# Kernel tuning notes

Hardware: AMD Instinct MI355X
Metric: run time of the kernel (lower is better)

The kernel has to match this reference:

```python
import jax, jax.numpy as jnp
import numpy as np
from jax import lax

B, S, T, E, H, V = 32, 64, 48, 512, 1024, 32000
PAD = 0


def lstm_cell(x, h, c, W_ih, W_hh, b_ih, b_hh):
    # PyTorch gate order: i, f, g, o
    gates = x @ W_ih.T + b_ih + h @ W_hh.T + b_hh
    i, f, g, o = jnp.split(gates, 4, axis=-1)
    c = jax.nn.sigmoid(f) * c + jax.nn.sigmoid(i) * jnp.tanh(g)
    h = jax.nn.sigmoid(o) * jnp.tanh(c)
    return h, c


def setup_inputs() -> dict:
    key = jax.random.key(0)
    ks = jax.random.split(key, 24)
    sc = 0.02
    n = lambda k, shape: jax.random.normal(k, shape, jnp.float32) * sc
    src_emb = n(ks[0], (V, E)).at[PAD].set(0.0)
    tgt_emb = n(ks[1], (V, E)).at[PAD].set(0.0)
    inp = {
        "input_sequences": jax.random.randint(ks[2], (B, S), 0, V),
        "target_sequences": jax.random.randint(ks[3], (B, T), 0, V),
        "src_emb": src_emb,
        "tgt_emb": tgt_emb,
        "enc_Wih_f": n(ks[4], (4 * H, E)),
        "enc_Whh_f": n(ks[5], (4 * H, H)),
        "enc_bih_f": n(ks[6], (4 * H,)),
        "enc_bhh_f": n(ks[7], (4 * H,)),
        "enc_Wih_b": n(ks[8], (4 * H, E)),
        "enc_Whh_b": n(ks[9], (4 * H, H)),
        "enc_bih_b": n(ks[10], (4 * H,)),
        "enc_bhh_b": n(ks[11], (4 * H,)),
        "dec_Wih": n(ks[12], (4 * H, E + H)),
        "dec_Whh": n(ks[13], (4 * H, H)),
        "dec_bih": n(ks[14], (4 * H,)),
        "dec_bhh": n(ks[15], (4 * H,)),
        "W_init_h": n(ks[16], (H, 2 * H)),
        "W_init_c": n(ks[17], (H, 2 * H)),
        "W_att": n(ks[18], (H, 2 * H)),
        "W_comb": n(ks[19], (H, 3 * H)),
        "W_proj": n(ks[20], (V, H)),
    }
    return inp


def reference(input_sequences, target_sequences, src_emb, tgt_emb,
              enc_Wih_f, enc_Whh_f, enc_bih_f, enc_bhh_f,
              enc_Wih_b, enc_Whh_b, enc_bih_b, enc_bhh_b,
              dec_Wih, dec_Whh, dec_bih, dec_bhh,
              W_init_h, W_init_c, W_att, W_comb, W_proj):
    bsz = input_sequences.shape[0]
    x_src = src_emb[input_sequences.T]  # (S, B, E) time-major

    def make_enc_step(W_ih, W_hh, b_ih, b_hh):
        def step(carry, x):
            h, c = carry
            h, c = lstm_cell(x, h, c, W_ih, W_hh, b_ih, b_hh)
            return (h, c), h
        return step

    h0 = jnp.zeros((bsz, H), x_src.dtype)
    c0 = jnp.zeros((bsz, H), x_src.dtype)
    # bidirectional encoder
    (hf, cf), hs_f = lax.scan(make_enc_step(enc_Wih_f, enc_Whh_f, enc_bih_f, enc_bhh_f), (h0, c0), x_src)
    (hb, cb), hs_b = lax.scan(make_enc_step(enc_Wih_b, enc_Whh_b, enc_bih_b, enc_bhh_b), (h0, c0), x_src[::-1])
    enc_h = jnp.concatenate([hs_f, hs_b[::-1]], axis=-1).transpose(1, 0, 2)  # (B, S, 2H)
    last_hidden = jnp.concatenate([hf, hb], axis=-1)  # (B, 2H)
    last_cell = jnp.concatenate([cf, cb], axis=-1)

    dec_h0 = last_hidden @ W_init_h.T
    dec_c0 = last_cell @ W_init_c.T
    enc_att = enc_h @ W_att.T  # (B, S, H)

    x_tgt = tgt_emb[target_sequences.T]  # (T, B, E)

    def dec_step(carry, e_t):
        h, c, prev_out = carry
        x = jnp.concatenate([e_t, prev_out], axis=-1)  # (B, E+H)
        h, c = lstm_cell(x, h, c, dec_Wih, dec_Whh, dec_bih, dec_bhh)
        scores = jnp.einsum('bh,bsh->bs', h, enc_att)
        attn = jax.nn.softmax(scores, axis=-1)
        ctx = jnp.einsum('bs,bsd->bd', attn, enc_h)  # (B, 2H)
        out = jnp.concatenate([h, ctx], axis=-1) @ W_comb.T  # (B, H)
        return (h, c, out), out

    prev0 = jnp.zeros((bsz, H), x_src.dtype)
    _, outs = lax.scan(dec_step, (dec_h0, dec_c0, prev0), x_tgt)  # (T, B, H)

    logits = outs @ W_proj.T  # (T, B, V)
    P = jax.nn.log_softmax(logits, axis=-1)
    tgt = target_sequences.T  # (T, B)
    # P[t] predicts tgt[t+1]; torch.gather with smaller index truncates P to T-1 steps
    gold = jnp.take_along_axis(P[:-1], tgt[1:][..., None], axis=-1)[..., 0]  # (T-1, B)
    scores = gold.sum(axis=0)  # (B,)
    return scores
```

## Files before the change

kernel.cpp:

```cpp
#include <hip/hip_runtime.h>

typedef short v8s __attribute__((ext_vector_type(8)));
typedef float v4f __attribute__((ext_vector_type(4)));
typedef unsigned short u16;

#define DI __device__ __forceinline__
#define MFMA(a, b, c) __builtin_amdgcn_mfma_f32_16x16x32_bf16(a, b, c, 0, 0, 0)

constexpr int B = 32, S = 64, T = 48, E = 512, H = 1024, V = 32000;
constexpr int TP = T - 1;
constexpr int MROWS = TP * B;
constexpr int NCH = 250;

DI u16 f2bf(float f) {
    unsigned u = __float_as_uint(f);
    unsigned r = (u + 0x7FFFu + ((u >> 16) & 1u)) >> 16;
    return (u16)r;
}
DI float bf2f(u16 h) { return __uint_as_float(((unsigned)h) << 16); }
DI v8s load8(const u16* p) { return *reinterpret_cast<const v8s*>(p); }

typedef __attribute__((address_space(1))) const unsigned int gu32;
typedef __attribute__((address_space(3))) unsigned int lu32;
DI void gload_lds16(const u16* g, u16* l) {
    __builtin_amdgcn_global_load_lds((gu32*)g, (lu32*)l, 16, 0, 0);
}

DI void cstore(unsigned* p, unsigned v) {
    __hip_atomic_store(p, v, __ATOMIC_RELAXED, __HIP_MEMORY_SCOPE_AGENT);
}
DI int cload(const int* p) {
    return __hip_atomic_load(p, __ATOMIC_RELAXED, __HIP_MEMORY_SCOPE_AGENT);
}

DI void gbar2(int* bar, int bid, int nblk, int v) {
    __syncthreads();
    if (bid == 0) {
        int t = threadIdx.x;
        if (t > 0 && t < nblk) {
            while (cload(bar + 16 + t * 4) < v) __builtin_amdgcn_s_sleep(1);
        }
        __syncthreads();
        if (t == 0)
            __hip_atomic_store(bar, v, __ATOMIC_RELAXED, __HIP_MEMORY_SCOPE_AGENT);
    } else {
        if (threadIdx.x == 0) {
            __hip_atomic_store(bar + 16 + bid * 4, v, __ATOMIC_RELAXED,
                               __HIP_MEMORY_SCOPE_AGENT);
            while (cload(bar) < v) __builtin_amdgcn_s_sleep(2);
        }
        __syncthreads();
    }
}

__global__ __launch_bounds__(256) void k_cvt(const float* __restrict__ s,
                                             u16* __restrict__ d, int n4) {
    int i = blockIdx.x * 256 + threadIdx.x;
    if (i >= n4) return;
    float4 v = reinterpret_cast<const float4*>(s)[i];
    ushort4 o;
    o.x = f2bf(v.x); o.y = f2bf(v.y); o.z = f2bf(v.z); o.w = f2bf(v.w);
    reinterpret_cast<ushort4*>(d)[i] = o;
}

struct CvtD {
    const float* src[11];
    u16* dst[11];
    int n4[11];
    int start[12];
};
__global__ __launch_bounds__(256) void k_cvtm(CvtD d) {
    int blk = blockIdx.x;
    int seg = 0;
    #pragma unroll
    for (int q = 0; q < 11; ++q)
        if (blk >= d.start[q + 1]) seg = q + 1;
    int i = (blk - d.start[seg]) * 256 + threadIdx.x;
    if (i >= d.n4[seg]) return;
    float4 v = reinterpret_cast<const float4*>(d.src[seg])[i];
    ushort4 o;
    o.x = f2bf(v.x); o.y = f2bf(v.y); o.z = f2bf(v.z); o.w = f2bf(v.w);
    reinterpret_cast<ushort4*>(d.dst[seg])[i] = o;
}

__global__ __launch_bounds__(256) void k_embed(const int* __restrict__ seq, int seqstr,
                                               int nsteps, const float* __restrict__ emb,
                                               u16* __restrict__ out) {
    int i = blockIdx.x * 256 + threadIdx.x;
    int total = nsteps * B * (E / 4);
    if (i >= total) return;
    int q = i & 127;
    int sb = i >> 7;
    int b = sb & 31;
    int s = sb >> 5;
    int tok = seq[b * seqstr + s];
    float4 v = reinterpret_cast<const float4*>(emb + (size_t)tok * E)[q];
    ushort4 o;
    o.x = f2bf(v.x); o.y = f2bf(v.y); o.z = f2bf(v.z); o.w = f2bf(v.w);
    reinterpret_cast<ushort4*>(out + ((size_t)(s * B + b)) * E)[q] = o;
}

__global__ __launch_bounds__(256) void k_ench(const u16* __restrict__ hsf,
                                              const u16* __restrict__ hsb,
                                              u16* __restrict__ ench) {
    int id = blockIdx.x * 256 + threadIdx.x;
    int d8 = id & 255; int s = (id >> 8) & 63; int b = id >> 14;
    int d0 = d8 * 8;
    const u16* src = (d0 < H) ? hsf + (((size_t)(s + 1) * B + b)) * H + d0
                              : hsb + (((size_t)(S - s) * B + b)) * H + (d0 - H);
    *reinterpret_cast<v8s*>(ench + ((size_t)b * S + s) * 2 * H + d0) = load8(src);
}

__global__ __launch_bounds__(256) void k_transp(const u16* __restrict__ in,
                                                u16* __restrict__ out, int K, int N) {
    __shared__ u16 t[64][72];
    int nt = blockIdx.x * 64, kt = blockIdx.y * 64;
    int tid = threadIdx.x;
    int r = tid >> 2, cq = (tid & 3) * 16;
    v8s v0 = load8(in + (size_t)(kt + r) * N + nt + cq);
    v8s v1 = load8(in + (size_t)(kt + r) * N + nt + cq + 8);
    #pragma unroll
    for (int e = 0; e < 8; ++e) { t[r][cq + e] = (u16)v0[e]; t[r][cq + 8 + e] = (u16)v1[e]; }
    __syncthreads();
    v8s o0, o1;
    #pragma unroll
    for (int e = 0; e < 8; ++e) { o0[e] = (short)t[cq + e][r]; o1[e] = (short)t[cq + 8 + e][r]; }
    *reinterpret_cast<v8s*>(out + (size_t)(nt + r) * K + kt + cq) = o0;
    *reinterpret_cast<v8s*>(out + (size_t)(nt + r) * K + kt + cq + 8) = o1;
}

__global__ __launch_bounds__(256) void k_tile(const u16* __restrict__ A, int astr,
                                              const u16* __restrict__ W, int wstr,
                                              float* __restrict__ outf,
                                              u16* __restrict__ outb, int ostr,
                                              int ktiles) {
    __shared__ __align__(16) u16 As[128 * 64];
    __shared__ __align__(16) u16 Bs[128 * 64];
    const int tid = threadIdx.x;
    const int lane = tid & 63, wv = tid >> 6;
    const int l15 = lane & 15, lg = lane >> 4;
    const int wr = wv >> 1, wc = wv & 1;
    const int m0 = blockIdx.y * 128, n0 = blockIdx.x * 128;
    const int srow = lane >> 3, sc_ = lane & 7;

    v4f acc[4][4];
    #pragma unroll
    for (int i = 0; i < 4; ++i)
        #pragma unroll
        for (int j = 0; j < 4; ++j) acc[i][j] = v4f{0.f, 0.f, 0.f, 0.f};

    for (int kt = 0; kt < ktiles; ++kt) {
        const int kb = kt * 64;
        #pragma unroll
        for (int i = 0; i < 4; ++i) {
            int chunk = wv * 4 + i;
            int row = chunk * 8 + srow;
            int csw = (sc_ ^ (row & 7)) << 3;
            gload_lds16(A + (size_t)(m0 + row) * astr + kb + csw, As + chunk * 512);
            gload_lds16(W + (size_t)(n0 + row) * wstr + kb + csw, Bs + chunk * 512);
        }
        __syncthreads();
        #pragma unroll
        for (int kk = 0; kk < 2; ++kk) {
            int sw = (((kk << 2) | lg) ^ (l15 & 7)) << 3;
            v8s af[4], bfv[4];
            #pragma unroll
            for (int mi = 0; mi < 4; ++mi)
                af[mi] = load8(As + (wr * 64 + mi * 16 + l15) * 64 + sw);
            #pragma unroll
            for (int ni = 0; ni < 4; ++ni)
                bfv[ni] = load8(Bs + (wc * 64 + ni * 16 + l15) * 64 + sw);
            #pragma unroll
            for (int mi = 0; mi < 4; ++mi)
                #pragma unroll
                for (int ni = 0; ni < 4; ++ni)
                    acc[mi][ni] = MFMA(af[mi], bfv[ni], acc[mi][ni]);
        }
        __syncthreads();
    }
    #pragma unroll
    for (int mi = 0; mi < 4; ++mi)
        #pragma unroll
        for (int rr = 0; rr < 4; ++rr) {
            int row = m0 + wr * 64 + mi * 16 + lg * 4 + rr;
            #pragma unroll
            for (int ni = 0; ni < 4; ++ni) {
                int col = n0 + wc * 64 + ni * 16 + l15;
                if (outf) outf[(size_t)row * ostr + col] = acc[mi][ni][rr];
                else      outb[(size_t)row * ostr + col] = f2bf(acc[mi][ni][rr]);
            }
        }
}

struct T4 {
    const u16* A[4]; int astr[4];
    const u16* W[4]; int wstr[4];
    float* outf[4]; u16* outb[4]; int ostr[4];
    int kt[4]; int nx[4]; int start[5];
};
__global__ __launch_bounds__(256) void k_tile4(T4 p) {
    __shared__ __align__(16) u16 As[128 * 64];
    __shared__ __align__(16) u16 Bs[128 * 64];
    int blk = blockIdx.x;
    int seg = 0;
    #pragma unroll
    for (int q = 0; q < 3; ++q)
        if (blk >= p.start[q + 1]) seg = q + 1;
    int lid = blk - p.start[seg];
    const int n0 = (lid % p.nx[seg]) * 128;
    const int m0 = (lid / p.nx[seg]) * 128;
    const u16* A = p.A[seg];
    const u16* W = p.W[seg];
    const int astr = p.astr[seg], wstr = p.wstr[seg], ostr = p.ostr[seg];
    float* outf = p.outf[seg];
    u16* outb = p.outb[seg];
    const int ktiles = p.kt[seg];
    const int tid = threadIdx.x;
    const int lane = tid & 63, wv = tid >> 6;
    const int l15 = lane & 15, lg = lane >> 4;
    const int wr = wv >> 1, wc = wv & 1;
    const int srow = lane >> 3, sc_ = lane & 7;

    v4f acc[4][4];
    #pragma unroll
    for (int i = 0; i < 4; ++i)
        #pragma unroll
        for (int j = 0; j < 4; ++j) acc[i][j] = v4f{0.f, 0.f, 0.f, 0.f};

    for (int kt = 0; kt < ktiles; ++kt) {
        const int kb = kt * 64;
        #pragma unroll
        for (int i = 0; i < 4; ++i) {
            int chunk = wv * 4 + i;
            int row = chunk * 8 + srow;
            int csw = (sc_ ^ (row & 7)) << 3;
            gload_lds16(A + (size_t)(m0 + row) * astr + kb + csw, As + chunk * 512);
            gload_lds16(W + (size_t)(n0 + row) * wstr + kb + csw, Bs + chunk * 512);
        }
        __syncthreads();
        #pragma unroll
        for (int kk = 0; kk < 2; ++kk) {
            int sw = (((kk << 2) | lg) ^ (l15 & 7)) << 3;
            v8s af[4], bfv[4];
            #pragma unroll
            for (int mi = 0; mi < 4; ++mi)
                af[mi] = load8(As + (wr * 64 + mi * 16 + l15) * 64 + sw);
            #pragma unroll
            for (int ni = 0; ni < 4; ++ni)
                bfv[ni] = load8(Bs + (wc * 64 + ni * 16 + l15) * 64 + sw);
            #pragma unroll
            for (int mi = 0; mi < 4; ++mi)
                #pragma unroll
                for (int ni = 0; ni < 4; ++ni)
                    acc[mi][ni] = MFMA(af[mi], bfv[ni], acc[mi][ni]);
        }
        __syncthreads();
    }
    #pragma unroll
    for (int mi = 0; mi < 4; ++mi)
        #pragma unroll
        for (int rr = 0; rr < 4; ++rr) {
            int row = m0 + wr * 64 + mi * 16 + lg * 4 + rr;
            #pragma unroll
            for (int ni = 0; ni < 4; ++ni) {
                int col = n0 + wc * 64 + ni * 16 + l15;
                if (outf) outf[(size_t)row * ostr + col] = acc[mi][ni][rr];
                else      outb[(size_t)row * ostr + col] = f2bf(acc[mi][ni][rr]);
            }
        }
}

struct Seg { const u16* a; int astr; const u16* w; int wstr; int k; };

__global__ __launch_bounds__(512) void k_mm(Seg s1, Seg s2, float* __restrict__ outf,
                                            u16* __restrict__ outb, int ostr, int ks,
                                            int sub) {
    const int tid = threadIdx.x;
    const int wv = tid >> 6, lane = tid & 63;
    const int l15 = lane & 15, lg = lane >> 4;
    const int wrow = blockIdx.x * 16 + l15;
    const int k0 = wv * ks, k1 = k0 + ks;
    v4f acc0 = {0.f, 0.f, 0.f, 0.f}, acc1 = {0.f, 0.f, 0.f, 0.f};
    int base = 0;
    auto doseg = [&](const Seg& sg) {
        if (sg.k == 0) return;
        int s0 = k0 > base ? k0 : base;
        int send = base + sg.k;
        int s1e = k1 < send ? k1 : send;
        const u16* wp = sg.w + (size_t)wrow * sg.wstr + 8 * lg;
        const u16* a0p = sg.a + (size_t)l15 * sg.astr + 8 * lg;
        const u16* a1p = sg.a + (size_t)(16 + l15) * sg.astr + 8 * lg;
        #pragma unroll 2
        for (int k = s0; k < s1e; k += 32) {
            int kl = k - base;
            v8s bf = load8(wp + kl);
            v8s af0 = load8(a0p + kl);
            v8s af1 = load8(a1p + kl);
            acc0 = MFMA(af0, bf, acc0);
            acc1 = MFMA(af1, bf, acc1);
        }
        base += sg.k;
    };
    doseg(s1); doseg(s2);

    __shared__ float g[8][32][16];
    #pragma unroll
    for (int r = 0; r < 4; ++r) {
        g[wv][lg * 4 + r][l15] = acc0[r];
        g[wv][16 + lg * 4 + r][l15] = acc1[r];
    }
    __syncthreads();
    {
        int b = tid >> 4, cl = tid & 15;
        float v = 0.f;
        #pragma unroll
        for (int w = 0; w < 8; ++w) v += g[w][b][cl];
        int col = blockIdx.x * 16 + cl;
        size_t idx = (size_t)b * ostr + col;
        if (outb)      outb[idx] = f2bf(v);
        else if (sub)  outf[idx] -= v;
        else           outf[idx] = v;
    }
}

__global__ __launch_bounds__(512) void k_enc(
    const float* __restrict__ xgF, const float* __restrict__ xgB,
    const u16* __restrict__ whhf, const u16* __restrict__ whhb,
    const float* __restrict__ bihF, const float* __restrict__ bhhF,
    const float* __restrict__ bihB, const float* __restrict__ bhhB,
    u16* __restrict__ hsf, u16* __restrict__ hsb,
    float* __restrict__ cfinal, int* __restrict__ bars) {
    const int blk = blockIdx.x;
    const int dir = blk >> 7, bid = blk & 127;
    const int tid = threadIdx.x;
    const u16* whh = dir ? whhb : whhf;
    const float* xg = dir ? xgB : xgF;
    const float* bih = dir ? bihB : bihF;
    const float* bhh = dir ? bhhB : bhhF;
    u16* hs = dir ? hsb : hsf;
    int* bar = bars + dir * 2048;
    const int j0 = bid * 8;
    __shared__ u16 wlds[32 * 1024];
    __shared__ float glds[8][32][34];
    __shared__ u16 htmp[32][8];
    {
        int r = tid >> 4, kc = tid & 15;
        int gate = r >> 3, jl = r & 7;
        const u16* src = whh + (size_t)(gate * H + j0 + jl) * H;
        #pragma unroll
        for (int i = 0; i < 8; ++i) {
            int c = kc + 16 * i;
            v8s v = load8(src + c * 8);
            *reinterpret_cast<v8s*>(wlds + r * 1024 + ((c ^ (r & 7)) * 8)) = v;
        }
    }
    float creg = 0.f;
    const int pb = tid >> 3, pj = tid & 7;
    float bsum[4];
    if (tid < 256) {
        #pragma unroll
        for (int gt = 0; gt < 4; ++gt)
            bsum[gt] = bih[gt * H + j0 + pj] + bhh[gt * H + j0 + pj];
    }
    __syncthreads();
    const int wv = tid >> 6, lane = tid & 63, l15 = lane & 15, lg = lane >> 4;
    for (int s = 0; s < S; ++s) {
        float xv[4];
        if (tid < 256) {
            int xrow = ((dir ? (S - 1 - s) : s) * 32 + pb) * 4096;
            const float* xr = xg + xrow + j0 + pj;
            #pragma unroll
            for (int gt = 0; gt < 4; ++gt) xv[gt] = xr[gt * H];
        }
        const u16* hp = hs + (size_t)s * (B * H);
        const u16* a0 = hp + (size_t)l15 * H + wv * 128 + 8 * lg;
        const u16* a1 = a0 + (size_t)16 * H;
        v4f acc00 = {0,0,0,0}, acc01 = {0,0,0,0}, acc10 = {0,0,0,0}, acc11 = {0,0,0,0};
        #pragma unroll
        for (int kb = 0; kb < 4; ++kb) {
            int c = wv * 16 + kb * 4 + lg;
            int w0 = l15;
            int w1 = 16 + l15;
            v8s bf0 = load8(wlds + w0 * 1024 + ((c ^ (w0 & 7)) * 8));
            v8s bf1 = load8(wlds + w1 * 1024 + ((c ^ (w1 & 7)) * 8));
            v8s af0 = load8(a0 + kb * 32);
            v8s af1 = load8(a1 + kb * 32);
            acc00 = MFMA(af0, bf0, acc00);
            acc10 = MFMA(af0, bf1, acc10);
            acc01 = MFMA(af1, bf0, acc01);
            acc11 = MFMA(af1, bf1, acc11);
        }
        #pragma unroll
        for (int r = 0; r < 4; ++r) {
            glds[wv][lg * 4 + r][l15] = acc00[r];
            glds[wv][lg * 4 + r][16 + l15] = acc10[r];
            glds[wv][16 + lg * 4 + r][l15] = acc01[r];
            glds[wv][16 + lg * 4 + r][16 + l15] = acc11[r];
        }
        __syncthreads();
        if (tid < 256) {
            float gv[4];
            #pragma unroll
            for (int gt = 0; gt < 4; ++gt) {
                float v = 0.f;
                #pragma unroll
                for (int w = 0; w < 8; ++w) v += glds[w][pb][gt * 8 + pj];
                gv[gt] = v + xv[gt] + bsum[gt];
            }
            float si = 1.f / (1.f + expf(-gv[0]));
            float sf = 1.f / (1.f + expf(-gv[1]));
            float tg = tanhf(gv[2]);
            float so = 1.f / (1.f + expf(-gv[3]));
            creg = sf * creg + si * tg;
            htmp[pb][pj] = f2bf(so * tanhf(creg));
        }
        __syncthreads();
        if (tid < 128) {
            int rb = tid >> 2, c2 = (tid & 3) * 2;
            unsigned val = (unsigned)htmp[rb][c2] | ((unsigned)htmp[rb][c2 + 1] << 16);
            cstore((unsigned*)(hs + (size_t)(s + 1) * (B * H) + (size_t)rb * H + j0 + c2), val);
        }
        if (s < S - 1) gbar2(bar, bid, 128, s + 1);
    }
    if (tid < 256) cfinal[(size_t)dir * B * H + (size_t)pb * H + j0 + pj] = creg;
}

__global__ __launch_bounds__(512) void k_dec(
    const float* __restrict__ xgD, const u16* __restrict__ dwhh,
    const u16* __restrict__ wfuse, const float* __restrict__ bih,
    const float* __restrict__ bhh, const float* __restrict__ decc,
    const u16* __restrict__ encab, const u16* __restrict__ ench,
    u16* __restrict__ hc, int* __restrict__ bar) {
    const int bid = blockIdx.x, tid = threadIdx.x;
    const int j0 = bid * 4;
    __shared__ u16 wlds[16 * 3072];
    __shared__ float glds[8][32][16];
    __shared__ float hl[1056];
    __shared__ float sc[64], aw[64];
    __shared__ float cpart[4][128][2];
    __shared__ u16 htmp[32][4];
    {
        int r = tid >> 5, kc = tid & 31;
        int gate = r >> 2, jl = r & 3;
        int grow = gate * H + j0 + jl;
        for (int i = 0; i < 12; ++i) {
            int c = kc + 32 * i;
            int k = c * 8;
            v8s wf = load8(wfuse + (size_t)grow * 3072 + k);
            if (k < 1024) {
                v8s wh = load8(dwhh + (size_t)grow * 1024 + k);
                #pragma unroll
                for (int e = 0; e < 8; ++e)
                    wf[e] = (short)f2bf(bf2f((u16)wf[e]) + bf2f((u16)wh[e]));
            }
            *reinterpret_cast<v8s*>(wlds + r * 3072 + ((c ^ (r & 7)) * 8)) = wf;
        }
    }
    const int pb = tid >> 2, pj = tid & 3;
    float creg = 0.f;
    float bsum[4];
    if (tid < 128) {
        creg = decc[(size_t)pb * H + j0 + pj];
        #pragma unroll
        for (int gt = 0; gt < 4; ++gt)
            bsum[gt] = bih[gt * H + j0 + pj] + bhh[gt * H + j0 + pj];
    }
    __syncthreads();
    const int wv = tid >> 6, lane = tid & 63, l15 = lane & 15, lg = lane >> 4;
    const int ab = bid >> 3, ach = bid & 7;
    for (int t = 0; t < T; ++t) {
        const u16* hp = hc + (size_t)t * (B * 3072);
        u16* hn = hc + (size_t)(t + 1) * (B * 3072);
        float xv[4];
        if (tid < 128) {
            const float* xr = xgD + (size_t)(t * 32 + pb) * 4096 + j0 + pj;
            #pragma unroll
            for (int gt = 0; gt < 4; ++gt) xv[gt] = xr[gt * H];
        }
        const u16* a0 = hp + (size_t)l15 * 3072 + wv * 384 + 8 * lg;
        const u16* a1 = a0 + (size_t)16 * 3072;
        v4f acc0 = {0.f, 0.f, 0.f, 0.f}, acc1 = {0.f, 0.f, 0.f, 0.f};
        #pragma unroll
        for (int kb = 0; kb < 12; ++kb) {
            int c = wv * 48 + kb * 4 + lg;
            v8s bf = load8(wlds + l15 * 3072 + ((c ^ (l15 & 7)) * 8));
            v8s af0 = load8(a0 + kb * 32);
            v8s af1 = load8(a1 + kb * 32);
            acc0 = MFMA(af0, bf, acc0);
            acc1 = MFMA(af1, bf, acc1);
        }
        #pragma unroll
        for (int r = 0; r < 4; ++r) {
            glds[wv][lg * 4 + r][l15] = acc0[r];
            glds[wv][16 + lg * 4 + r][l15] = acc1[r];
        }
        __syncthreads();
        if (tid < 128) {
            float gv[4];
            #pragma unroll
            for (int gt = 0; gt < 4; ++gt) {
                float v = 0.f;
                #pragma unroll
                for (int w = 0; w < 8; ++w) v += glds[w][pb][gt * 4 + pj];
                gv[gt] = v + xv[gt] + bsum[gt];
            }
            float si = 1.f / (1.f + expf(-gv[0]));
            float sf = 1.f / (1.f + expf(-gv[1]));
            float tg = tanhf(gv[2]);
            float so = 1.f / (1.f + expf(-gv[3]));
            creg = sf * creg + si * tg;
            htmp[pb][pj] = f2bf(so * tanhf(creg));
        }
        __syncthreads();
        if (tid < 64) {
            int rb = tid >> 1, c2 = (tid & 1) * 2;
            unsigned val = (unsigned)htmp[rb][c2] | ((unsigned)htmp[rb][c2 + 1] << 16);
            cstore((unsigned*)(hn + (size_t)rb * 3072 + j0 + c2), val);
        }
        gbar2(bar, bid, 256, 2 * t + 1);
        {
            const u16* hb = hn + (size_t)ab * 3072;
            for (int i = tid; i < 1024; i += 512)
                hl[((i >> 7) * 132) + (i & 127)] = bf2f(hb[i]);
            __syncthreads();
            {
                int si2 = tid >> 3, pt = tid & 7;
                const u16* ap = encab + ((size_t)(ab * 64 + si2)) * 1024 + pt * 128;
                const float* hq = hl + pt * 132;
                float ps = 0.f;
                #pragma unroll
                for (int x = 0; x < 16; ++x) {
                    v8s v = load8(ap + x * 8);
                    #pragma unroll
                    for (int e = 0; e < 8; ++e) ps += bf2f((u16)v[e]) * hq[x * 8 + e];
                }
                ps += __shfl_xor(ps, 1); ps += __shfl_xor(ps, 2); ps += __shfl_xor(ps, 4);
                if (pt == 0) sc[si2] = ps;
            }
            __syncthreads();
            if (tid < 64) {
                float v = sc[tid];
                float m = v;
                #pragma unroll
                for (int o = 32; o; o >>= 1) m = fmaxf(m, __shfl_xor(m, o));
                float e = expf(v - m), sum = e;
                #pragma unroll
                for (int o = 32; o; o >>= 1) sum += __shfl_xor(sum, o);
                aw[tid] = e / sum;
            }
            __syncthreads();
            {
                int q = tid >> 7, dp = tid & 127;
                int d = ach * 256 + dp * 2;
                const u16* ep = ench + (size_t)ab * S * 2048 + (size_t)(q * 16) * 2048 + d;
                float c0 = 0.f, c1 = 0.f;
                #pragma unroll 8
                for (int s2 = 0; s2 < 16; ++s2) {
                    unsigned uv = *reinterpret_cast<const unsigned*>(ep);
                    float w = aw[q * 16 + s2];
                    c0 += w * bf2f((u16)(uv & 0xFFFF));
                    c1 += w * bf2f((u16)(uv >> 16));
                    ep += 2048;
                }
                cpart[q][dp][0] = c0;
                cpart[q][dp][1] = c1;
            }
            __syncthreads();
            if (tid < 128) {
                float c0 = cpart[0][tid][0] + cpart[1][tid][0]
                         + cpart[2][tid][0] + cpart[3][tid][0];
                float c1 = cpart[0][tid][1] + cpart[1][tid][1]
                         + cpart[2][tid][1] + cpart[3][tid][1];
                unsigned ov = ((unsigned)f2bf(c1) << 16) | f2bf(c0);
                cstore((unsigned*)(hn + (size_t)ab * 3072 + 1024 + ach * 256 + tid * 2), ov);
            }
        }
        if (t < T - 1) gbar2(bar, bid, 256, 2 * t + 2);
    }
}

__global__ __launch_bounds__(512) void k_proj(const u16* __restrict__ A,
                                              const u16* __restrict__ W,
                                              const int* __restrict__ tgt,
                                              float* __restrict__ pmax,
                                              float* __restrict__ psum,
                                              float* __restrict__ pgold) {
    __shared__ __align__(16) u16 As[256 * 64];
    __shared__ __align__(16) u16 Bs[128 * 64];
    __shared__ float red[256][2][3];
    const int tid = threadIdx.x;
    const int lane = tid & 63, wv = tid >> 6;
    const int l15 = lane & 15, lg = lane >> 4;
    const int wr = wv >> 1, wc = wv & 1;
    int orig = blockIdx.x;
    int xcd = orig & 7, loc = orig >> 3;
    int wgid = (xcd < 4 ? xcd * 188 : 752 + (xcd - 4) * 187) + loc;
    int nt = wgid / 6, mt = wgid % 6;
    const int m0 = mt * 256, n0 = nt * 128;
    const int srow = lane >> 3, sc_ = lane & 7;

    v4f acc[4][4];
    #pragma unroll
    for (int i = 0; i < 4; ++i)
        #pragma unroll
        for (int j = 0; j < 4; ++j) acc[i][j] = v4f{0.f, 0.f, 0.f, 0.f};

    for (int kt = 0; kt < 16; ++kt) {
        const int kb = kt * 64;
        #pragma unroll
        for (int i = 0; i < 4; ++i) {
            int chunk = wv * 4 + i;
            int row = chunk * 8 + srow;
            int csw = (sc_ ^ (row & 7)) << 3;
            gload_lds16(A + (size_t)(m0 + row) * 1024 + kb + csw, As + chunk * 512);
        }
        #pragma unroll
        for (int i = 0; i < 2; ++i) {
            int chunk = wv * 2 + i;
            int row = chunk * 8 + srow;
            int csw = (sc_ ^ (row & 7)) << 3;
            gload_lds16(W + (size_t)(n0 + row) * 1024 + kb + csw, Bs + chunk * 512);
        }
        __syncthreads();
        #pragma unroll
        for (int kk = 0; kk < 2; ++kk) {
            int sw = (((kk << 2) | lg) ^ (l15 & 7)) << 3;
            v8s af[4], bfv[4];
            #pragma unroll
            for (int mi = 0; mi < 4; ++mi)
                af[mi] = load8(As + (wr * 64 + mi * 16 + l15) * 64 + sw);
            #pragma unroll
            for (int ni = 0; ni < 4; ++ni)
                bfv[ni] = load8(Bs + (wc * 64 + ni * 16 + l15) * 64 + sw);
            #pragma unroll
            for (int mi = 0; mi < 4; ++mi)
                #pragma unroll
                for (int ni = 0; ni < 4; ++ni)
                    acc[mi][ni] = MFMA(af[mi], bfv[ni], acc[mi][ni]);
        }
        __syncthreads();
    }
    #pragma unroll
    for (int mi = 0; mi < 4; ++mi) {
        #pragma unroll
        for (int rr = 0; rr < 4; ++rr) {
            int lrow = wr * 64 + mi * 16 + lg * 4 + rr;
            int grow = m0 + lrow;
            float vmax = -1e30f;
            #pragma unroll
            for (int ni = 0; ni < 4; ++ni) vmax = fmaxf(vmax, acc[mi][ni][rr]);
            #pragma unroll
            for (int x = 1; x < 16; x <<= 1) vmax = fmaxf(vmax, __shfl_xor(vmax, x));
            float se = 0.f;
            #pragma unroll
            for (int ni = 0; ni < 4; ++ni) se += expf(acc[mi][ni][rr] - vmax);
            #pragma unroll
            for (int x = 1; x < 16; x <<= 1) se += __shfl_xor(se, x);
            int t = grow >> 5, b = grow & 31;
            int g = (grow < MROWS) ? tgt[b * T + t + 1] : -1;
            float gv = 0.f;
            #pragma unroll
            for (int ni = 0; ni < 4; ++ni) {
                int col = n0 + wc * 64 + ni * 16 + l15;
                if (col == g) gv = acc[mi][ni][rr];
            }
            #pragma unroll
            for (int x = 1; x < 16; x <<= 1) gv += __shfl_xor(gv, x);
            if (l15 == 0) {
                red[lrow][wc][0] = vmax;
                red[lrow][wc][1] = se;
                red[lrow][wc][2] = gv;
            }
        }
    }
    __syncthreads();
    if (tid < 256) {
        int grow = m0 + tid;
        if (grow < MROWS) {
            float ma = red[tid][0][0], mb = red[tid][1][0];
            float M = fmaxf(ma, mb);
            float Sv = red[tid][0][1] * expf(ma - M) + red[tid][1][1] * expf(mb - M);
            float G = red[tid][0][2] + red[tid][1][2];
            size_t idx = (size_t)grow * NCH + nt;
            pmax[idx] = M; psum[idx] = Sv; pgold[idx] = G;
        }
    }
}

__global__ __launch_bounds__(256) void k_lse(const float* __restrict__ pmax,
                                             const float* __restrict__ psum,
                                             const float* __restrict__ pgold,
                                             float* __restrict__ logP) {
    int item = blockIdx.x * 4 + (threadIdx.x >> 6);
    int lane = threadIdx.x & 63;
    if (item >= MROWS) return;
    float m = -1e30f, g = 0.f;
    for (int c = lane; c < NCH; c += 64) {
        size_t idx = (size_t)item * NCH + c;
        m = fmaxf(m, pmax[idx]);
        g += pgold[idx];
    }
    for (int o = 32; o; o >>= 1) m = fmaxf(m, __shfl_xor(m, o));
    float s = 0.f;
    for (int c = lane; c < NCH; c += 64) {
        size_t idx = (size_t)item * NCH + c;
        s += psum[idx] * expf(pmax[idx] - m);
    }
    for (int o = 32; o; o >>= 1) { s += __shfl_xor(s, o); g += __shfl_xor(g, o); }
    if (lane == 0) logP[item] = g - (m + logf(s));
}

__global__ __launch_bounds__(64) void k_final(const float* __restrict__ logP,
                                              float* __restrict__ out) {
    int b = threadIdx.x;
    if (b < 32) {
        float s = 0.f;
        for (int t = 0; t < TP; ++t) s += logP[t * 32 + b];
        out[b] = s;
    }
}

extern "C" void kernel_launch(void* const* d_in, const int* in_sizes, int n_in,
                              void* d_out, int out_size, void* d_ws, size_t ws_size,
                              hipStream_t stream) {
    const int*   seq_in  = (const int*)d_in[0];
    const int*   seq_tgt = (const int*)d_in[1];
    const float* src_emb = (const float*)d_in[2];
    const float* tgt_emb = (const float*)d_in[3];
    const float* eWihF = (const float*)d_in[4];
    const float* eWhhF = (const float*)d_in[5];
    const float* eBihF = (const float*)d_in[6];
    const float* eBhhF = (const float*)d_in[7];
    const float* eWihB = (const float*)d_in[8];
    const float* eWhhB = (const float*)d_in[9];
    const float* eBihB = (const float*)d_in[10];
    const float* eBhhB = (const float*)d_in[11];
    const float* dWih  = (const float*)d_in[12];
    const float* dWhh  = (const float*)d_in[13];
    const float* dBih  = (const float*)d_in[14];
    const float* dBhh  = (const float*)d_in[15];
    const float* WinH  = (const float*)d_in[16];
    const float* WinC  = (const float*)d_in[17];
    const float* Watt  = (const float*)d_in[18];
    const float* Wcomb = (const float*)d_in[19];
    const float* Wproj = (const float*)d_in[20];

    char* ws = (char*)d_ws;
    size_t off = 0;
    auto alloc = [&](size_t bytes) -> char* {
        off = (off + 255) & ~(size_t)255;
        char* p = ws + off;
        off += bytes;
        return p;
    };
    const size_t G4 = 4 * (size_t)H;
    const size_t slot = (size_t)B * H;
    u16* wihf = (u16*)alloc(G4 * E * 2);
    u16* whhf = (u16*)alloc(G4 * H * 2);
    u16* wihb = (u16*)alloc(G4 * E * 2);
    u16* whhb = (u16*)alloc(G4 * H * 2);
    u16* dwih = (u16*)alloc(G4 * (E + H) * 2);
    u16* dwhh = (u16*)alloc(G4 * H * 2);
    u16* winh = (u16*)alloc((size_t)H * 2 * H * 2);
    u16* winc = (u16*)alloc((size_t)H * 2 * H * 2);
    u16* watt = (u16*)alloc((size_t)H * 2 * H * 2);
    u16* wcmb = (u16*)alloc((size_t)H * 3 * H * 2);
    u16* wprj = (u16*)alloc((size_t)V * H * 2);
    u16* wcmbT = (u16*)alloc((size_t)3 * H * H * 2);
    u16* wfuse = (u16*)alloc((size_t)G4 * 3 * H * 2);
    u16* xsrc  = (u16*)alloc((size_t)S * B * E * 2);
    u16* xtgt  = (u16*)alloc((size_t)T * B * E * 2);
    u16* hsf   = (u16*)alloc((size_t)(S + 1) * slot * 2);
    u16* hsb   = (u16*)alloc((size_t)(S + 1) * slot * 2);
    u16* ench  = (u16*)alloc((size_t)B * S * 2 * H * 2);
    u16* encab = (u16*)alloc((size_t)B * S * H * 2);
    u16* hc    = (u16*)alloc((size_t)(T + 1) * B * 3072 * 2);
    u16* outsb = (u16*)alloc((size_t)(T * B) * H * 2);
    u16* lcbf  = (u16*)alloc(2 * slot * 2);
    float* xgF  = (float*)alloc((size_t)S * B * G4 * 4);
    float* xgB  = (float*)alloc((size_t)S * B * G4 * 4);
    float* xgD  = (float*)alloc((size_t)T * B * G4 * 4);
    float* cf2  = (float*)alloc(2 * slot * 4);
    float* decc = (float*)alloc(slot * 4);
    float* pmax  = (float*)alloc((size_t)MROWS * NCH * 4);
    float* psum  = (float*)alloc((size_t)MROWS * NCH * 4);
    float* pgold = (float*)alloc((size_t)MROWS * NCH * 4);
    float* logP  = (float*)alloc((size_t)MROWS * 4);
    int* bars = (int*)alloc(3 * 2048 * 4);
    (void)ws_size; (void)in_sizes; (void)n_in; (void)out_size;

    hipMemsetAsync(hsf, 0, slot * 2, stream);
    hipMemsetAsync(hsb, 0, slot * 2, stream);
    hipMemsetAsync(hc, 0, (size_t)B * 3072 * 2, stream);
    hipMemsetAsync(bars, 0, 3 * 2048 * 4, stream);

    {
        CvtD d;
        const float* srcs[11] = {eWihF, eWhhF, eWihB, eWhhB, dWih, dWhh,
                                 WinH, WinC, Watt, Wcomb, Wproj};
        u16* dsts[11] = {wihf, whhf, wihb, whhb, dwih, dwhh,
                         winh, winc, watt, wcmb, wprj};
        size_t ns[11] = {G4 * E, G4 * H, G4 * E, G4 * H, G4 * (E + H), G4 * H,
                         (size_t)H * 2 * H, (size_t)H * 2 * H, (size_t)H * 2 * H,
                         (size_t)H * 3 * H, (size_t)V * H};
        int blk = 0;
        for (int i = 0; i < 11; ++i) {
            d.src[i] = srcs[i];
            d.dst[i] = dsts[i];
            d.n4[i] = (int)(ns[i] / 4);
            d.start[i] = blk;
            blk += (d.n4[i] + 255) / 256;
        }
        d.start[11] = blk;
        k_cvtm<<<dim3(blk), dim3(256), 0, stream>>>(d);
    }

    k_embed<<<dim3((S * B * (E / 4) + 255) / 256), dim3(256), 0, stream>>>(
        seq_in, S, S, src_emb, xsrc);
    k_embed<<<dim3((T * B * (E / 4) + 255) / 256), dim3(256), 0, stream>>>(
        seq_tgt, T, T, tgt_emb, xtgt);

    k_transp<<<dim3(3 * H / 64, H / 64), dim3(256), 0, stream>>>(wcmb, wcmbT, H, 3 * H);

    {
        T4 p;
        p.A[0] = xsrc; p.astr[0] = E; p.W[0] = wihf; p.wstr[0] = E;
        p.outf[0] = xgF; p.outb[0] = nullptr; p.ostr[0] = 4096; p.kt[0] = 8; p.nx[0] = 32;
        p.A[1] = xsrc; p.astr[1] = E; p.W[1] = wihb; p.wstr[1] = E;
        p.outf[1] = xgB; p.outb[1] = nullptr; p.ostr[1] = 4096; p.kt[1] = 8; p.nx[1] = 32;
        p.A[2] = xtgt; p.astr[2] = E; p.W[2] = dwih; p.wstr[2] = E + H;
        p.outf[2] = xgD; p.outb[2] = nullptr; p.ostr[2] = 4096; p.kt[2] = 8; p.nx[2] = 32;
        p.A[3] = dwih + E; p.astr[3] = E + H; p.W[3] = wcmbT; p.wstr[3] = H;
        p.outf[3] = nullptr; p.outb[3] = wfuse; p.ostr[3] = 3 * H; p.kt[3] = 16; p.nx[3] = 24;
        p.start[0] = 0;
        p.start[1] = 512;
        p.start[2] = 1024;
        p.start[3] = 1408;
        p.start[4] = 1408 + 768;
        k_tile4<<<dim3(p.start[4]), dim3(256), 0, stream>>>(p);
    }

    k_enc<<<dim3(256), dim3(512), 0, stream>>>(xgF, xgB, whhf, whhb,
                                               eBihF, eBhhF, eBihB, eBhhB,
                                               hsf, hsb, cf2, bars);

    k_ench<<<dim3(B * S * (2 * H / 8) / 256), dim3(256), 0, stream>>>(hsf, hsb, ench);
    k_tile<<<dim3(8, 16), dim3(256), 0, stream>>>(ench, 2 * H, watt, 2 * H,
                                                  nullptr, encab, H, 32);
    {
        int n4 = (int)(2 * slot / 4);
        k_cvt<<<dim3((n4 + 255) / 256), dim3(256), 0, stream>>>(cf2, lcbf, n4);
    }

    {
        Seg a1{hsf + (size_t)S * slot, H, winh, 2 * H, H};
        Seg a2{hsb + (size_t)S * slot, H, winh + H, 2 * H, H};
        k_mm<<<dim3(H / 16), dim3(512), 0, stream>>>(a1, a2, nullptr, hc, 3072,
                                                     2 * H / 8, 0);
        Seg c1{lcbf, H, winc, 2 * H, H};
        Seg c2{lcbf + slot, H, winc + H, 2 * H, H};
        k_mm<<<dim3(H / 16), dim3(512), 0, stream>>>(c1, c2, decc, nullptr, H,
                                                     2 * H / 8, 0);
        Seg f1{hc, 3072, wfuse, 3 * H, H};
        Seg f0{nullptr, 0, nullptr, 0, 0};
        k_mm<<<dim3(G4 / 16), dim3(512), 0, stream>>>(f1, f0, xgD, nullptr, 4096,
                                                      H / 8, 1);
    }

    k_dec<<<dim3(256), dim3(512), 0, stream>>>(xgD, dwhh, wfuse, dBih, dBhh, decc,
                                               encab, ench, hc, bars + 4096);

    k_tile<<<dim3(8, 12), dim3(256), 0, stream>>>(hc + B * 3072, 3 * H, wcmb, 3 * H,
                                                  nullptr, outsb, H, 48);

    k_proj<<<dim3(1500), dim3(512), 0, stream>>>(outsb, wprj, seq_tgt, pmax, psum, pgold);
    k_lse<<<dim3((MROWS + 3) / 4), dim3(256), 0, stream>>>(pmax, psum, pgold, logP);
    k_final<<<dim3(1), dim3(64), 0, stream>>>(logP, (float*)d_out);
}
```

Before: 1.385 ms.

## Fold attention context through precomputed encoder-weight products in decoder recurrence

Instead of computing the attention context per step and feeding it through the fused gate weights, the decoder precomputes enc_h times the context part of the fused weights (encWT) and enc_h times W_comb's context part (encWc). Each step then only needs attention weights times these folded matrices, which removes the per-step context reduction over 2H and shrinks the recurrent matmul K from 3072 to 1024. Attention is now computed by only 32 blocks, and weights go through a global buffer. The output combination is split into a separate k_outs pass plus a smaller GEMM with an added fp32 term. The cost is extra precompute GEMMs and more LDS per block, plus rounding changes from folding in bf16.

```diff
diff --git a/kernel.cpp b/kernel.cpp
--- a/kernel.cpp
+++ b/kernel.cpp
@@ -133,7 +133,8 @@
                                               const u16* __restrict__ W, int wstr,
                                               float* __restrict__ outf,
                                               u16* __restrict__ outb, int ostr,
-                                              int ktiles) {
+                                              int ktiles,
+                                              const float* __restrict__ addf) {
     __shared__ __align__(16) u16 As[128 * 64];
     __shared__ __align__(16) u16 Bs[128 * 64];
     const int tid = threadIdx.x;
@@ -186,8 +187,11 @@
             #pragma unroll
             for (int ni = 0; ni < 4; ++ni) {
                 int col = n0 + wc * 64 + ni * 16 + l15;
-                if (outf) outf[(size_t)row * ostr + col] = acc[mi][ni][rr];
-                else      outb[(size_t)row * ostr + col] = f2bf(acc[mi][ni][rr]);
+                size_t idx = (size_t)row * ostr + col;
+                float v = acc[mi][ni][rr];
+                if (addf) v += addf[idx];
+                if (outf) outf[idx] = v;
+                else      outb[idx] = f2bf(v);
             }
         }
 }
@@ -427,33 +431,41 @@
 
 __global__ __launch_bounds__(512) void k_dec(
     const float* __restrict__ xgD, const u16* __restrict__ dwhh,
-    const u16* __restrict__ wfuse, const float* __restrict__ bih,
-    const float* __restrict__ bhh, const float* __restrict__ decc,
-    const u16* __restrict__ encab, const u16* __restrict__ ench,
-    u16* __restrict__ hc, int* __restrict__ bar) {
+    const u16* __restrict__ wfuse, const u16* __restrict__ encWT,
+    const float* __restrict__ bih, const float* __restrict__ bhh,
+    const float* __restrict__ decc, const u16* __restrict__ encab,
+    u16* __restrict__ hst, float* __restrict__ awst, int* __restrict__ bar) {
     const int bid = blockIdx.x, tid = threadIdx.x;
     const int j0 = bid * 4;
-    __shared__ u16 wlds[16 * 3072];
+    __shared__ u16 wdh[16 * 1024];
+    __shared__ u16 encw[16 * 2048];
     __shared__ float glds[8][32][16];
+    __shared__ float awl[2048];
+    __shared__ float foldl[32][18];
     __shared__ float hl[1056];
-    __shared__ float sc[64], aw[64];
-    __shared__ float cpart[4][128][2];
+    __shared__ float sc[64];
     __shared__ u16 htmp[32][4];
     {
         int r = tid >> 5, kc = tid & 31;
         int gate = r >> 2, jl = r & 3;
         int grow = gate * H + j0 + jl;
-        for (int i = 0; i < 12; ++i) {
+        #pragma unroll
+        for (int i = 0; i < 4; ++i) {
             int c = kc + 32 * i;
-            int k = c * 8;
-            v8s wf = load8(wfuse + (size_t)grow * 3072 + k);
-            if (k < 1024) {
-                v8s wh = load8(dwhh + (size_t)grow * 1024 + k);
-                #pragma unroll
-                for (int e = 0; e < 8; ++e)
-                    wf[e] = (short)f2bf(bf2f((u16)wf[e]) + bf2f((u16)wh[e]));
-            }
-            *reinterpret_cast<v8s*>(wlds + r * 3072 + ((c ^ (r & 7)) * 8)) = wf;
+            v8s wf = load8(wfuse + (size_t)grow * 3072 + c * 8);
+            v8s wh = load8(dwhh + (size_t)grow * 1024 + c * 8);
+            #pragma unroll
+            for (int e = 0; e < 8; ++e)
+                wf[e] = (short)f2bf(bf2f((u16)wf[e]) + bf2f((u16)wh[e]));
+            *reinterpret_cast<v8s*>(wdh + r * 1024 + ((c ^ (r & 7)) * 8)) = wf;
+        }
+    }
+    {
+        for (int chunk = tid; chunk < 4096; chunk += 512) {
+            int r = chunk >> 8, g = chunk & 255;
+            int grow = (r >> 2) * H + j0 + (r & 3);
+            v8s v = load8(encWT + (size_t)grow * 2048 + g * 8);
+            *reinterpret_cast<v8s*>(encw + r * 2048 + (g & 7) * 256 + (g >> 3) * 8) = v;
         }
     }
     const int pb = tid >> 2, pj = tid & 3;
@@ -467,23 +479,24 @@
     }
     __syncthreads();
     const int wv = tid >> 6, lane = tid & 63, l15 = lane & 15, lg = lane >> 4;
-    const int ab = bid >> 3, ach = bid & 7;
+    const int fr = tid >> 5, fb = tid & 31;
     for (int t = 0; t < T; ++t) {
-        const u16* hp = hc + (size_t)t * (B * 3072);
-        u16* hn = hc + (size_t)(t + 1) * (B * 3072);
+        const u16* hp = hst + (size_t)t * (B * H);
+        u16* hn = hst + (size_t)(t + 1) * (B * H);
+        for (int i = tid; i < 2048; i += 512) awl[i] = awst[(size_t)t * 2048 + i];
         float xv[4];
         if (tid < 128) {
             const float* xr = xgD + (size_t)(t * 32 + pb) * 4096 + j0 + pj;
             #pragma unroll
             for (int gt = 0; gt < 4; ++gt) xv[gt] = xr[gt * H];
         }
-        const u16* a0 = hp + (size_t)l15 * 3072 + wv * 384 + 8 * lg;
-        const u16* a1 = a0 + (size_t)16 * 3072;
+        const u16* a0 = hp + (size_t)l15 * H + wv * 128 + 8 * lg;
+        const u16* a1 = a0 + (size_t)16 * H;
         v4f acc0 = {0.f, 0.f, 0.f, 0.f}, acc1 = {0.f, 0.f, 0.f, 0.f};
         #pragma unroll
-        for (int kb = 0; kb < 12; ++kb) {
-            int c = wv * 48 + kb * 4 + lg;
-            v8s bf = load8(wlds + l15 * 3072 + ((c ^ (l15 & 7)) * 8));
+        for (int kb = 0; kb < 4; ++kb) {
+            int c = wv * 16 + kb * 4 + lg;
+            v8s bf = load8(wdh + l15 * 1024 + ((c ^ (l15 & 7)) * 8));
             v8s af0 = load8(a0 + kb * 32);
             v8s af1 = load8(a1 + kb * 32);
             acc0 = MFMA(af0, bf, acc0);
@@ -495,11 +508,24 @@
             glds[wv][16 + lg * 4 + r][l15] = acc1[r];
         }
         __syncthreads();
+        {
+            float f = 0.f;
+            const u16* ew = encw + fr * 2048 + fb * 8;
+            const float* ap = awl + fb * 64;
+            #pragma unroll
+            for (int sblk = 0; sblk < 8; ++sblk) {
+                v8s v = load8(ew + sblk * 256);
+                #pragma unroll
+                for (int e = 0; e < 8; ++e) f += ap[sblk * 8 + e] * bf2f((u16)v[e]);
+            }
+            foldl[fb][fr] = f;
+        }
+        __syncthreads();
         if (tid < 128) {
             float gv[4];
             #pragma unroll
             for (int gt = 0; gt < 4; ++gt) {
-                float v = 0.f;
+                float v = foldl[pb][gt * 4 + pj];
                 #pragma unroll
                 for (int w = 0; w < 8; ++w) v += glds[w][pb][gt * 4 + pj];
                 gv[gt] = v + xv[gt] + bsum[gt];
@@ -515,17 +541,17 @@
         if (tid < 64) {
             int rb = tid >> 1, c2 = (tid & 1) * 2;
             unsigned val = (unsigned)htmp[rb][c2] | ((unsigned)htmp[rb][c2 + 1] << 16);
-            cstore((unsigned*)(hn + (size_t)rb * 3072 + j0 + c2), val);
+            cstore((unsigned*)(hn + (size_t)rb * H + j0 + c2), val);
         }
         gbar2(bar, bid, 256, 2 * t + 1);
-        {
-            const u16* hb = hn + (size_t)ab * 3072;
+        if (bid < 32) {
+            int b = bid;
             for (int i = tid; i < 1024; i += 512)
-                hl[((i >> 7) * 132) + (i & 127)] = bf2f(hb[i]);
+                hl[((i >> 7) * 132) + (i & 127)] = bf2f(hn[(size_t)b * H + i]);
             __syncthreads();
             {
                 int si2 = tid >> 3, pt = tid & 7;
-                const u16* ap = encab + ((size_t)(ab * 64 + si2)) * 1024 + pt * 128;
+                const u16* ap = encab + ((size_t)(b * 64 + si2)) * 1024 + pt * 128;
                 const float* hq = hl + pt * 132;
                 float ps = 0.f;
                 #pragma unroll
@@ -546,36 +572,35 @@
                 float e = expf(v - m), sum = e;
                 #pragma unroll
                 for (int o = 32; o; o >>= 1) sum += __shfl_xor(sum, o);
-                aw[tid] = e / sum;
+                cstore((unsigned*)(awst + (size_t)(t + 1) * 2048 + b * 64 + tid),
+                       __float_as_uint(e / sum));
             }
-            __syncthreads();
-            {
-                int q = tid >> 7, dp = tid & 127;
-                int d = ach * 256 + dp * 2;
-                const u16* ep = ench + (size_t)ab * S * 2048 + (size_t)(q * 16) * 2048 + d;
-                float c0 = 0.f, c1 = 0.f;
-                #pragma unroll 8
-                for (int s2 = 0; s2 < 16; ++s2) {
-                    unsigned uv = *reinterpret_cast<const unsigned*>(ep);
-                    float w = aw[q * 16 + s2];
-                    c0 += w * bf2f((u16)(uv & 0xFFFF));
-                    c1 += w * bf2f((u16)(uv >> 16));
-                    ep += 2048;
-                }
-                cpart[q][dp][0] = c0;
-                cpart[q][dp][1] = c1;
-            }
-            __syncthreads();
-            if (tid < 128) {
-                float c0 = cpart[0][tid][0] + cpart[1][tid][0]
-                         + cpart[2][tid][0] + cpart[3][tid][0];
-                float c1 = cpart[0][tid][1] + cpart[1][tid][1]
-                         + cpart[2][tid][1] + cpart[3][tid][1];
-                unsigned ov = ((unsigned)f2bf(c1) << 16) | f2bf(c0);
-                cstore((unsigned*)(hn + (size_t)ab * 3072 + 1024 + ach * 256 + tid * 2), ov);
-            }
         }
         if (t < T - 1) gbar2(bar, bid, 256, 2 * t + 2);
+    }
+}
+
+__global__ __launch_bounds__(256) void k_outs(const float* __restrict__ awst,
+                                              const u16* __restrict__ encWc,
+                                              float* __restrict__ outctx) {
+    int b = blockIdx.x;
+    __shared__ float awsh[64];
+    int c0 = threadIdx.x * 4;
+    for (int t = 0; t < T; ++t) {
+        if (threadIdx.x < 64)
+            awsh[threadIdx.x] = awst[(size_t)(t + 1) * 2048 + b * 64 + threadIdx.x];
+        __syncthreads();
+        float a0 = 0.f, a1 = 0.f, a2 = 0.f, a3 = 0.f;
+        for (int s = 0; s < 64; ++s) {
+            float w = awsh[s];
+            ushort4 v = *reinterpret_cast<const ushort4*>(
+                encWc + ((size_t)(b * 64 + s)) * 1024 + c0);
+            a0 += w * bf2f(v.x); a1 += w * bf2f(v.y);
+            a2 += w * bf2f(v.z); a3 += w * bf2f(v.w);
+        }
+        float4 o{a0, a1, a2, a3};
+        *reinterpret_cast<float4*>(outctx + ((size_t)(t * 32 + b)) * 1024 + c0) = o;
+        __syncthreads();
     }
 }
 
@@ -768,13 +793,15 @@
     u16* wprj = (u16*)alloc((size_t)V * H * 2);
     u16* wcmbT = (u16*)alloc((size_t)3 * H * H * 2);
     u16* wfuse = (u16*)alloc((size_t)G4 * 3 * H * 2);
+    u16* encWT = (u16*)alloc((size_t)G4 * 2048 * 2);
+    u16* encWc = (u16*)alloc((size_t)2048 * H * 2);
     u16* xsrc  = (u16*)alloc((size_t)S * B * E * 2);
     u16* xtgt  = (u16*)alloc((size_t)T * B * E * 2);
     u16* hsf   = (u16*)alloc((size_t)(S + 1) * slot * 2);
     u16* hsb   = (u16*)alloc((size_t)(S + 1) * slot * 2);
     u16* ench  = (u16*)alloc((size_t)B * S * 2 * H * 2);
     u16* encab = (u16*)alloc((size_t)B * S * H * 2);
-    u16* hc    = (u16*)alloc((size_t)(T + 1) * B * 3072 * 2);
+    u16* hst   = (u16*)alloc((size_t)(T + 1) * slot * 2);
     u16* outsb = (u16*)alloc((size_t)(T * B) * H * 2);
     u16* lcbf  = (u16*)alloc(2 * slot * 2);
     float* xgF  = (float*)alloc((size_t)S * B * G4 * 4);
@@ -782,6 +809,8 @@
     float* xgD  = (float*)alloc((size_t)T * B * G4 * 4);
     float* cf2  = (float*)alloc(2 * slot * 4);
     float* decc = (float*)alloc(slot * 4);
+    float* awst = (float*)alloc((size_t)(T + 1) * 2048 * 4);
+    float* outctx = (float*)alloc((size_t)(T * B) * H * 4);
     float* pmax  = (float*)alloc((size_t)MROWS * NCH * 4);
     float* psum  = (float*)alloc((size_t)MROWS * NCH * 4);
     float* pgold = (float*)alloc((size_t)MROWS * NCH * 4);
@@ -791,7 +820,7 @@
 
     hipMemsetAsync(hsf, 0, slot * 2, stream);
     hipMemsetAsync(hsb, 0, slot * 2, stream);
-    hipMemsetAsync(hc, 0, (size_t)B * 3072 * 2, stream);
+    hipMemsetAsync(awst, 0, 2048 * 4, stream);
     hipMemsetAsync(bars, 0, 3 * 2048 * 4, stream);
 
     {
@@ -846,7 +875,11 @@
 
     k_ench<<<dim3(B * S * (2 * H / 8) / 256), dim3(256), 0, stream>>>(hsf, hsb, ench);
     k_tile<<<dim3(8, 16), dim3(256), 0, stream>>>(ench, 2 * H, watt, 2 * H,
-                                                  nullptr, encab, H, 32);
+                                                  nullptr, encab, H, 32, nullptr);
+    k_tile<<<dim3(16, 32), dim3(256), 0, stream>>>(wfuse + H, 3 * H, ench, 2 * H,
+                                                   nullptr, encWT, 2048, 32, nullptr);
+    k_tile<<<dim3(8, 16), dim3(256), 0, stream>>>(ench, 2 * H, wcmb + H, 3 * H,
+                                                  nullptr, encWc, H, 32, nullptr);
     {
         int n4 = (int)(2 * slot / 4);
         k_cvt<<<dim3((n4 + 255) / 256), dim3(256), 0, stream>>>(cf2, lcbf, n4);
@@ -855,23 +888,24 @@
     {
         Seg a1{hsf + (size_t)S * slot, H, winh, 2 * H, H};
         Seg a2{hsb + (size_t)S * slot, H, winh + H, 2 * H, H};
-        k_mm<<<dim3(H / 16), dim3(512), 0, stream>>>(a1, a2, nullptr, hc, 3072,
+        k_mm<<<dim3(H / 16), dim3(512), 0, stream>>>(a1, a2, nullptr, hst, H,
                                                      2 * H / 8, 0);
         Seg c1{lcbf, H, winc, 2 * H, H};
         Seg c2{lcbf + slot, H, winc + H, 2 * H, H};
         k_mm<<<dim3(H / 16), dim3(512), 0, stream>>>(c1, c2, decc, nullptr, H,
                                                      2 * H / 8, 0);
-        Seg f1{hc, 3072, wfuse, 3 * H, H};
+        Seg f1{hst, H, wfuse, 3 * H, H};
         Seg f0{nullptr, 0, nullptr, 0, 0};
         k_mm<<<dim3(G4 / 16), dim3(512), 0, stream>>>(f1, f0, xgD, nullptr, 4096,
                                                       H / 8, 1);
     }
 
-    k_dec<<<dim3(256), dim3(512), 0, stream>>>(xgD, dwhh, wfuse, dBih, dBhh, decc,
-                                               encab, ench, hc, bars + 4096);
-
-    k_tile<<<dim3(8, 12), dim3(256), 0, stream>>>(hc + B * 3072, 3 * H, wcmb, 3 * H,
-                                                  nullptr, outsb, H, 48);
+    k_dec<<<dim3(256), dim3(512), 0, stream>>>(xgD, dwhh, wfuse, encWT, dBih, dBhh,
+                                               decc, encab, hst, awst, bars + 4096);
+
+    k_outs<<<dim3(32), dim3(256), 0, stream>>>(awst, encWc, outctx);
+    k_tile<<<dim3(8, 12), dim3(256), 0, stream>>>(hst + slot, H, wcmb, 3 * H,
+                                                  nullptr, outsb, H, 16, outctx);
 
     k_proj<<<dim3(1500), dim3(512), 0, stream>>>(outsb, wprj, seq_tgt, pmax, psum, pgold);
     k_lse<<<dim3((MROWS + 3) / 4), dim3(256), 0, stream>>>(pmax, psum, pgold, logP);
```

New measurement: 1.739 ms. 1.26x slower.
